# Optimization experiments

Hardware: AMD Instinct MI355X
Metric: run time of the kernel (lower is better)

The kernel has to match this reference:

```python
import jax, jax.numpy as jnp
import numpy as np

B, N, C, H = 8, 1024, 1024, 16
D = C // H
SCALE = D ** -0.5


def setup_inputs() -> dict:
    key = jax.random.key(0)
    ks = jax.random.split(key, 5)
    s = 0.02  # keep pre-softmax logits in a sane range
    return {
        "x": jax.random.normal(ks[0], (B, N, C), dtype=jnp.float32),
        "Wq": jax.random.normal(ks[1], (C, C), dtype=jnp.float32) * s,
        "bq": jax.random.normal(ks[2], (C,), dtype=jnp.float32) * s,
        "Wkv": jax.random.normal(ks[3], (C, 2 * C), dtype=jnp.float32) * s,
        "bkv": jax.random.normal(ks[4], (2 * C,), dtype=jnp.float32) * s,
    }


def reference(x, Wq, bq, Wkv, bkv):
    b, n, c = x.shape
    h, d = H, c // H
    q = (x @ Wq + bq).reshape(b, n, h, d)                 # [b,n,h,d]
    kv = x @ Wkv + bkv                                     # [b,n,2c]
    k, v = jnp.split(kv, 2, axis=-1)                       # each [b,n,c]
    k = k.reshape(b, n, h, d)
    v = v.reshape(b, n, h, d)
    att = jnp.einsum("bnhd,bmhd->bnmh", q, k) * SCALE      # [b,n,m,h]
    att = jax.nn.softmax(att, axis=2)                      # softmax over keys (m)
    out = jnp.einsum("bnmh,bmhd->bnhd", att, v).reshape(b, n, c)
    return out
```

## Files before the change

kernel.cpp:

```cpp
#include <hip/hip_runtime.h>
#include <stdint.h>

using u16 = unsigned short;
using u32 = unsigned int;
using bf16x8 = __attribute__((ext_vector_type(8))) __bf16;
using f32x4  = __attribute__((ext_vector_type(4))) float;

#define NB 8
#define NN 1024
#define NC 1024
#define NH 16
#define ND 64
#define QSCALE 0.18033688011112042f

__device__ __forceinline__ u16 f2bf(float f) {
  u32 u = __float_as_uint(f);
  return (u16)((u + 0x7fffu + ((u >> 16) & 1u)) >> 16);
}
__device__ __forceinline__ u16 bfc(float f) {
  __bf16 b = (__bf16)f;
  return __builtin_bit_cast(u16, b);
}
__device__ __forceinline__ u32 pack2(u16 a, u16 b) { return (u32)a | ((u32)b << 16); }

__device__ __forceinline__ void gload16(const void* g, void* l) {
  __builtin_amdgcn_global_load_lds((__attribute__((address_space(1))) const u32*)g,
                                   (__attribute__((address_space(3))) u32*)l, 16, 0, 0);
}

__global__ void k_prep(const float* __restrict__ x, const float* __restrict__ Wq,
                       const float* __restrict__ Wkv,
                       u16* __restrict__ xb, u16* __restrict__ Wt) {
  __shared__ u16 tile[64][72];
  int bid = blockIdx.x;
  int t = threadIdx.x;
  if (bid < 8192) {
    int i = bid * 256 + t;
    float4 v = ((const float4*)x)[i];
    ((uint2*)xb)[i] = make_uint2(pack2(f2bf(v.x), f2bf(v.y)), pack2(f2bf(v.z), f2bf(v.w)));
    return;
  }
  {
    int pb = bid - 8192;
    int k0 = (pb & 15) << 6;
    int c0 = (pb >> 4) << 6;
    bool isQ = (c0 < 1024);
    const float* src = isQ ? Wq : Wkv;
    int ldw  = isQ ? 1024 : 2048;
    int csrc = isQ ? c0 : (c0 - 1024);
    float sc = isQ ? QSCALE : 1.0f;

    int r  = t >> 2;
    int cq = (t & 3) << 4;
    const float* p = src + (size_t)(k0 + r) * ldw + csrc + cq;
#pragma unroll
    for (int j = 0; j < 16; j += 4) {
      float4 v = *(const float4*)(p + j);
      tile[r][cq + j + 0] = f2bf(v.x * sc);
      tile[r][cq + j + 1] = f2bf(v.y * sc);
      tile[r][cq + j + 2] = f2bf(v.z * sc);
      tile[r][cq + j + 3] = f2bf(v.w * sc);
    }
    __syncthreads();
    int co = t >> 2;
    int kq = (t & 3) << 4;
    u16 v0[16];
#pragma unroll
    for (int j = 0; j < 16; ++j) v0[j] = tile[kq + j][co];
    uint4 o0, o1;
    o0.x = pack2(v0[0], v0[1]);  o0.y = pack2(v0[2], v0[3]);
    o0.z = pack2(v0[4], v0[5]);  o0.w = pack2(v0[6], v0[7]);
    o1.x = pack2(v0[8], v0[9]);  o1.y = pack2(v0[10], v0[11]);
    o1.z = pack2(v0[12], v0[13]); o1.w = pack2(v0[14], v0[15]);
    u16* dst = Wt + (size_t)(c0 + co) * 1024 + k0 + kq;
    *(uint4*)dst = o0;
    *(uint4*)(dst + 8) = o1;
  }
}

__launch_bounds__(512, 2)
__global__ void k_gemm(const u16* __restrict__ A, const u16* __restrict__ Bw,
                       const float* __restrict__ bq, const float* __restrict__ bkv,
                       u16* __restrict__ qws, u16* __restrict__ kws, u16* __restrict__ vtw) {
  __shared__ __align__(16) u16 LA[2][16384];
  __shared__ __align__(16) u16 LB[2][12288];
  int flat = blockIdx.x;
  int xcd = flat & 7, idx = flat >> 3;
  int m0 = (xcd * 4 + (idx & 3)) * 256;
  int n0 = (idx >> 2) * 192;
  int tid = threadIdx.x;
  int w = tid >> 6, lane = tid & 63;
  int lo = lane & 15, hi = lane >> 4;
  int wm = w >> 2, wn = w & 3;

  f32x4 acc[8][3] = {};

  int cs = ((tid & 7) ^ ((tid >> 3) & 7)) * 8;
  const u16* Ag = A  + (size_t)(m0 + (tid >> 3)) * 1024 + cs;
  const u16* Bg = Bw + (size_t)(n0 + (tid >> 3)) * 1024 + cs;

  int ck0 = ((hi ^ (lo & 7)) << 3);
  int ck1 = (((4 + hi) ^ (lo & 7)) << 3);
  const u16* laR = &LA[0][wm * 8192 + lo * 64];
  const u16* lbR = &LB[0][(wn * 48 + lo) * 64];

#define MFMA_(a, b, c) __builtin_amdgcn_mfma_f32_16x16x32_bf16(a, b, c, 0, 0, 0)
#define SBAR() __builtin_amdgcn_sched_barrier(0); __builtin_amdgcn_s_barrier(); __builtin_amdgcn_sched_barrier(0)
#define LGKM0() asm volatile("s_waitcnt lgkmcnt(0)" ::: "memory"); __builtin_amdgcn_sched_barrier(0)

#define ST_AH(BUF, MH, KT)                                                                     \
  gload16(Ag + (size_t)((MH) * 128) * 1024 + (KT) * 64,      &LA[BUF][(MH) * 8192 + tid * 8]); \
  gload16(Ag + (size_t)((MH) * 128 + 64) * 1024 + (KT) * 64, &LA[BUF][(MH) * 8192 + 4096 + tid * 8]);
#define ST_BT(BUF, NH, KT)                                                                     \
  gload16(Bg + (size_t)((NH) * 64) * 1024 + (KT) * 64,       &LB[BUF][(NH) * 4096 + tid * 8]);

#define QUAD(Q, NI)                                                           \
  __builtin_amdgcn_s_setprio(1);                                              \
  _Pragma("unroll")                                                           \
  for (int ks = 0; ks < 2; ++ks)                                              \
    _Pragma("unroll")                                                         \
    for (int mi = 0; mi < 4; ++mi)                                            \
      acc[(Q) * 4 + mi][NI] = MFMA_(af[mi][ks], bfr[NI][ks], acc[(Q) * 4 + mi][NI]); \
  __builtin_amdgcn_s_setprio(0);

  ST_AH(0, 0, 0); ST_AH(0, 1, 0); ST_BT(0, 0, 0); ST_BT(0, 1, 0); ST_BT(0, 2, 0);
  ST_AH(1, 0, 1); ST_AH(1, 1, 1); ST_BT(1, 0, 1); ST_BT(1, 1, 1); ST_BT(1, 2, 1);
  asm volatile("s_waitcnt vmcnt(7)" ::: "memory");
  __builtin_amdgcn_s_barrier();

#pragma unroll 1
  for (int t = 0; t < 16; ++t) {
    int b = t & 1;
    const u16* la = laR + b * 16384;
    const u16* lb = lbR + b * 12288;
    bf16x8 af[4][2], bfr[3][2];
    bool st = (t < 14);

#pragma unroll
    for (int mi = 0; mi < 4; ++mi) {
      af[mi][0] = *(const bf16x8*)(la + mi * 1024 + ck0);
      af[mi][1] = *(const bf16x8*)(la + mi * 1024 + ck1);
    }
    bfr[0][0] = *(const bf16x8*)(lb + ck0);
    bfr[0][1] = *(const bf16x8*)(lb + ck1);
    SBAR();
    LGKM0();
    QUAD(0, 0);
    SBAR();

    bfr[1][0] = *(const bf16x8*)(lb + 1024 + ck0);
    bfr[1][1] = *(const bf16x8*)(lb + 1024 + ck1);
    SBAR();
    LGKM0();
    QUAD(0, 1);
    SBAR();

    bfr[2][0] = *(const bf16x8*)(lb + 2048 + ck0);
    bfr[2][1] = *(const bf16x8*)(lb + 2048 + ck1);
    SBAR();
    LGKM0();
    QUAD(0, 2);
    SBAR();

#pragma unroll
    for (int mi = 0; mi < 4; ++mi) {
      af[mi][0] = *(const bf16x8*)(la + (4 + mi) * 1024 + ck0);
      af[mi][1] = *(const bf16x8*)(la + (4 + mi) * 1024 + ck1);
    }
    if (st) { ST_BT(b, 0, t + 2); }
    SBAR();
    LGKM0();
    QUAD(1, 0);
    SBAR();

    if (st) { ST_AH(b, 0, t + 2); ST_BT(b, 1, t + 2); }
    SBAR();
    QUAD(1, 1);
    SBAR();

    if (st) { ST_AH(b, 1, t + 2); ST_BT(b, 2, t + 2); }
    SBAR();
    QUAD(1, 2);
    if (t < 14)       { asm volatile("s_waitcnt vmcnt(7)" ::: "memory"); }
    else if (t == 14) { asm volatile("s_waitcnt vmcnt(0)" ::: "memory"); }
    SBAR();
  }
#undef QUAD
#undef ST_AH
#undef ST_BT
#undef SBAR
#undef LGKM0
#undef MFMA_

#pragma unroll
  for (int ni = 0; ni < 3; ++ni) {
    int c = n0 + wn * 48 + ni * 16 + lo;
    float bvl = (c < 1024) ? bq[c] * QSCALE : bkv[c - 1024];
    if (c < 2048) {
#pragma unroll
      for (int mi = 0; mi < 8; ++mi) {
#pragma unroll
        for (int r = 0; r < 4; ++r) {
          int m = m0 + wm * 128 + mi * 16 + hi * 4 + r;
          int b = m >> 10, tok = m & 1023;
          u16 o = f2bf(acc[mi][ni][r] + bvl);
          if (c < 1024) {
            int h = c >> 6, d = c & 63;
            qws[((size_t)(b * 16 + h) * 1024 + tok) * 64 + d] = o;
          } else {
            int c2 = c - 1024; int h = c2 >> 6, d = c2 & 63;
            kws[((size_t)(b * 16 + h) * 1024 + tok) * 64 + d] = o;
          }
        }
      }
    } else {
      int c2 = c - 2048; int h = c2 >> 6, d = c2 & 63;
#pragma unroll
      for (int mi = 0; mi < 8; ++mi) {
        int m = m0 + wm * 128 + mi * 16 + hi * 4;
        int b = m >> 10, tok = m & 1023;
        ushort4 pk;
        pk.x = bfc(acc[mi][ni][0] + bvl);
        pk.y = bfc(acc[mi][ni][1] + bvl);
        pk.z = bfc(acc[mi][ni][2] + bvl);
        pk.w = bfc(acc[mi][ni][3] + bvl);
        *(ushort4*)&vtw[((size_t)(b * 16 + h) * 64 + d) * 1024 + tok] = pk;
      }
    }
  }
}

__launch_bounds__(512)
__global__ void k_attn(const u16* __restrict__ q, const u16* __restrict__ k,
                       const u16* __restrict__ vt, float* __restrict__ out) {
  __shared__ __align__(16) u16 Ks[2][4096];
  __shared__ __align__(16) u16 Vs[2][4096];
  __shared__ __align__(16) u16 P[2][8][16][72];
  int bh = blockIdx.x;
  int q0 = blockIdx.y * 256;
  int tid = threadIdx.x;
  int w = tid >> 6, lane = tid & 63;
  int lo = lane & 15, hi = lane >> 4;
  int b = bh >> 4, h = bh & 15;

  const u16* kbase = k  + (size_t)bh * 65536;
  const u16* vbase = vt + (size_t)bh * 65536;

  int srow = w * 8 + (lane >> 3);
  int cg   = (lane & 7) ^ ((lane >> 3) & 7);
  const u16* gK = kbase + (size_t)srow * 64   + cg * 8;
  const u16* gV = vbase + (size_t)srow * 1024 + cg * 8;
  u16* lK0 = &Ks[0][w * 512];
  u16* lK1 = &Ks[1][w * 512];
  u16* lV0 = &Vs[0][w * 512];
  u16* lV1 = &Vs[1][w * 512];

  const u16* qp = q + ((size_t)bh * 1024 + q0 + w * 16 + lo) * 64 + hi * 8;
  bf16x8 qfA0 = *(const bf16x8*)(qp);
  bf16x8 qfA1 = *(const bf16x8*)(qp + 32);
  bf16x8 qfB0 = *(const bf16x8*)(qp + 128 * 64);
  bf16x8 qfB1 = *(const bf16x8*)(qp + 128 * 64 + 32);

  f32x4 accA[4] = {}, accB[4] = {};
  float mA = -1e30f, lA = 0.f;
  float mB = -1e30f, lB = 0.f;

  int sw = lo & 7;

  gload16(gK, lK0);
  gload16(gV, lV0);
  __syncthreads();

  for (int t = 0; t < 16; ++t) {
    int cur = t & 1;
    if (t < 15) {
      gload16(gK + (t + 1) * 4096, cur ? lK0 : lK1);
      gload16(gV + (t + 1) * 64,   cur ? lV0 : lV1);
    }
    f32x4 sA[4] = {}, sB[4] = {};
    const u16* kb = Ks[cur];
    __builtin_amdgcn_s_setprio(1);
#pragma unroll
    for (int ni = 0; ni < 4; ++ni) {
      const u16* kp = kb + (ni * 16 + lo) * 64;
      bf16x8 kf0 = *(const bf16x8*)(kp + ((hi ^ sw) * 8));
      bf16x8 kf1 = *(const bf16x8*)(kp + (((4 + hi) ^ sw) * 8));
      sA[ni] = __builtin_amdgcn_mfma_f32_16x16x32_bf16(kf0, qfA0, sA[ni], 0, 0, 0);
      sA[ni] = __builtin_amdgcn_mfma_f32_16x16x32_bf16(kf1, qfA1, sA[ni], 0, 0, 0);
      sB[ni] = __builtin_amdgcn_mfma_f32_16x16x32_bf16(kf0, qfB0, sB[ni], 0, 0, 0);
      sB[ni] = __builtin_amdgcn_mfma_f32_16x16x32_bf16(kf1, qfB1, sB[ni], 0, 0, 0);
    }
    __builtin_amdgcn_s_setprio(0);

#define SOFTMAX(S, M, L, PI)                                                   \
    {                                                                          \
      float a0 = fmaxf(fmaxf(S[0][0], S[0][1]), fmaxf(S[0][2], S[0][3]));      \
      float a1 = fmaxf(fmaxf(S[1][0], S[1][1]), fmaxf(S[1][2], S[1][3]));      \
      float a2 = fmaxf(fmaxf(S[2][0], S[2][1]), fmaxf(S[2][2], S[2][3]));      \
      float a3 = fmaxf(fmaxf(S[3][0], S[3][1]), fmaxf(S[3][2], S[3][3]));      \
      float pm = fmaxf(fmaxf(a0, a1), fmaxf(a2, a3));                          \
      pm = fmaxf(pm, __shfl_xor(pm, 16));                                      \
      pm = fmaxf(pm, __shfl_xor(pm, 32));                                      \
      if (!__all(pm <= M + 8.0f)) {                                            \
        float mn = fmaxf(M, pm);                                               \
        float corr = __builtin_amdgcn_exp2f(M - mn);                           \
        M = mn;                                                                \
        L *= corr;                                                             \
        float cr[4];                                                           \
        _Pragma("unroll")                                                      \
        for (int r = 0; r < 4; ++r) cr[r] = __shfl(corr, hi * 4 + r);          \
        _Pragma("unroll")                                                      \
        for (int ci = 0; ci < 4; ++ci)                                         \
          _Pragma("unroll")                                                    \
          for (int r = 0; r < 4; ++r) acc##PI[ci][r] *= cr[r];                 \
      }                                                                        \
      float rs = 0.f;                                                          \
      _Pragma("unroll")                                                        \
      for (int ni = 0; ni < 4; ++ni) {                                         \
        float p0 = __builtin_amdgcn_exp2f(S[ni][0] - M);                       \
        float p1 = __builtin_amdgcn_exp2f(S[ni][1] - M);                       \
        float p2 = __builtin_amdgcn_exp2f(S[ni][2] - M);                       \
        float p3 = __builtin_amdgcn_exp2f(S[ni][3] - M);                       \
        rs += (p0 + p1) + (p2 + p3);                                           \
        ushort4 pk;                                                            \
        pk.x = bfc(p0); pk.y = bfc(p1); pk.z = bfc(p2); pk.w = bfc(p3);        \
        *(ushort4*)&P[PI##I][w][lo][ni * 16 + hi * 4] = pk;                    \
      }                                                                        \
      rs += __shfl_xor(rs, 16);                                                \
      rs += __shfl_xor(rs, 32);                                                \
      L += rs;                                                                 \
    }
#define AI 0
#define BI 1
    SOFTMAX(sA, mA, lA, A)
    SOFTMAX(sB, mB, lB, B)
#undef SOFTMAX

    bf16x8 pA0 = *(const bf16x8*)(&P[0][w][lo][hi * 8]);
    bf16x8 pA1 = *(const bf16x8*)(&P[0][w][lo][32 + hi * 8]);
    bf16x8 pB0 = *(const bf16x8*)(&P[1][w][lo][hi * 8]);
    bf16x8 pB1 = *(const bf16x8*)(&P[1][w][lo][32 + hi * 8]);
    const u16* vb = Vs[cur];
    __builtin_amdgcn_s_setprio(1);
#pragma unroll
    for (int ci = 0; ci < 4; ++ci) {
      const u16* vp = vb + (ci * 16 + lo) * 64;
      bf16x8 vf0 = *(const bf16x8*)(vp + ((hi ^ sw) * 8));
      bf16x8 vf1 = *(const bf16x8*)(vp + (((4 + hi) ^ sw) * 8));
      accA[ci] = __builtin_amdgcn_mfma_f32_16x16x32_bf16(pA0, vf0, accA[ci], 0, 0, 0);
      accA[ci] = __builtin_amdgcn_mfma_f32_16x16x32_bf16(pA1, vf1, accA[ci], 0, 0, 0);
      accB[ci] = __builtin_amdgcn_mfma_f32_16x16x32_bf16(pB0, vf0, accB[ci], 0, 0, 0);
      accB[ci] = __builtin_amdgcn_mfma_f32_16x16x32_bf16(pB1, vf1, accB[ci], 0, 0, 0);
    }
    __builtin_amdgcn_s_setprio(0);
    __syncthreads();
  }
  {
    float inv = 1.0f / lA;
    float ivr[4];
#pragma unroll
    for (int r = 0; r < 4; ++r) ivr[r] = __shfl(inv, hi * 4 + r);
#pragma unroll
    for (int r = 0; r < 4; ++r) {
      int n = q0 + w * 16 + hi * 4 + r;
      float* dst = out + ((size_t)(b * 1024 + n)) * 1024 + h * 64;
#pragma unroll
      for (int ci = 0; ci < 4; ++ci) dst[ci * 16 + lo] = accA[ci][r] * ivr[r];
    }
  }
  {
    float inv = 1.0f / lB;
    float ivr[4];
#pragma unroll
    for (int r = 0; r < 4; ++r) ivr[r] = __shfl(inv, hi * 4 + r);
#pragma unroll
    for (int r = 0; r < 4; ++r) {
      int n = q0 + 128 + w * 16 + hi * 4 + r;
      float* dst = out + ((size_t)(b * 1024 + n)) * 1024 + h * 64;
#pragma unroll
      for (int ci = 0; ci < 4; ++ci) dst[ci * 16 + lo] = accB[ci][r] * ivr[r];
    }
  }
}

extern "C" void kernel_launch(void* const* d_in, const int* in_sizes, int n_in,
                              void* d_out, int out_size, void* d_ws, size_t ws_size,
                              hipStream_t stream) {
  const float* x   = (const float*)d_in[0];
  const float* Wq  = (const float*)d_in[1];
  const float* bq  = (const float*)d_in[2];
  const float* Wkv = (const float*)d_in[3];
  const float* bkv = (const float*)d_in[4];
  float* out = (float*)d_out;

  char* ws = (char*)d_ws;
  u16*   xb   = (u16*)(ws);
  u16*   Wt   = (u16*)(ws + 16777216);
  u16*   qws  = (u16*)(ws + 23080960);
  u16*   kws  = (u16*)(ws + 39858176);
  u16*   vtw  = (u16*)(ws + 73412608);

  k_prep<<<8960, 256, 0, stream>>>(x, Wq, Wkv, xb, Wt);
  k_gemm<<<512, 512, 0, stream>>>(xb, Wt, bq, bkv, qws, kws, vtw);
  {
    dim3 g(128, 4);
    k_attn<<<g, 512, 0, stream>>>(qws, kws, vtw, out);
  }
}
```

Before: 132.5 us.

## Enlarge QKV GEMM tile to 256x384 with interleaved single-stage prefetch

Doubles the N-tile of the projection GEMM from 192 to 384 columns, so each block computes 256x384 with 48 accumulators per lane, and halves the grid to 256 blocks. The K-loop pipeline is rebuilt: the next k-tile's global-to-LDS loads are spread across the MFMA groups of the current tile, with a full vmcnt(0) wait at the end of each iteration instead of the previous two-tile-ahead staggered prefetch. The goal is higher arithmetic intensity per LDS/global byte. In exchange, LDS use grows to about 160KB and register pressure rises, which could cut occupancy. With 256 blocks on 256 CUs there is only one wave of work and no latency hiding across blocks.

```diff
diff --git a/kernel.cpp b/kernel.cpp
--- a/kernel.cpp
+++ b/kernel.cpp
@@ -83,17 +83,17 @@
                        const float* __restrict__ bq, const float* __restrict__ bkv,
                        u16* __restrict__ qws, u16* __restrict__ kws, u16* __restrict__ vtw) {
   __shared__ __align__(16) u16 LA[2][16384];
-  __shared__ __align__(16) u16 LB[2][12288];
+  __shared__ __align__(16) u16 LB[2][24576];
   int flat = blockIdx.x;
   int xcd = flat & 7, idx = flat >> 3;
   int m0 = (xcd * 4 + (idx & 3)) * 256;
-  int n0 = (idx >> 2) * 192;
+  int n0 = (idx >> 2) * 384;
   int tid = threadIdx.x;
   int w = tid >> 6, lane = tid & 63;
   int lo = lane & 15, hi = lane >> 4;
   int wm = w >> 2, wn = w & 3;
 
-  f32x4 acc[8][3] = {};
+  f32x4 acc[8][6] = {};
 
   int cs = ((tid & 7) ^ ((tid >> 3) & 7)) * 8;
   const u16* Ag = A  + (size_t)(m0 + (tid >> 3)) * 1024 + cs;
@@ -101,100 +101,71 @@
 
   int ck0 = ((hi ^ (lo & 7)) << 3);
   int ck1 = (((4 + hi) ^ (lo & 7)) << 3);
-  const u16* laR = &LA[0][wm * 8192 + lo * 64];
-  const u16* lbR = &LB[0][(wn * 48 + lo) * 64];
+  const u16* laR = &LA[0][(wm * 128 + lo) * 64];
+  const u16* lbR = &LB[0][(wn * 96 + lo) * 64];
 
 #define MFMA_(a, b, c) __builtin_amdgcn_mfma_f32_16x16x32_bf16(a, b, c, 0, 0, 0)
 #define SBAR() __builtin_amdgcn_sched_barrier(0); __builtin_amdgcn_s_barrier(); __builtin_amdgcn_sched_barrier(0)
 #define LGKM0() asm volatile("s_waitcnt lgkmcnt(0)" ::: "memory"); __builtin_amdgcn_sched_barrier(0)
 
-#define ST_AH(BUF, MH, KT)                                                                     \
-  gload16(Ag + (size_t)((MH) * 128) * 1024 + (KT) * 64,      &LA[BUF][(MH) * 8192 + tid * 8]); \
-  gload16(Ag + (size_t)((MH) * 128 + 64) * 1024 + (KT) * 64, &LA[BUF][(MH) * 8192 + 4096 + tid * 8]);
-#define ST_BT(BUF, NH, KT)                                                                     \
-  gload16(Bg + (size_t)((NH) * 64) * 1024 + (KT) * 64,       &LB[BUF][(NH) * 4096 + tid * 8]);
-
-#define QUAD(Q, NI)                                                           \
-  __builtin_amdgcn_s_setprio(1);                                              \
-  _Pragma("unroll")                                                           \
-  for (int ks = 0; ks < 2; ++ks)                                              \
-    _Pragma("unroll")                                                         \
-    for (int mi = 0; mi < 4; ++mi)                                            \
-      acc[(Q) * 4 + mi][NI] = MFMA_(af[mi][ks], bfr[NI][ks], acc[(Q) * 4 + mi][NI]); \
-  __builtin_amdgcn_s_setprio(0);
-
-  ST_AH(0, 0, 0); ST_AH(0, 1, 0); ST_BT(0, 0, 0); ST_BT(0, 1, 0); ST_BT(0, 2, 0);
-  ST_AH(1, 0, 1); ST_AH(1, 1, 1); ST_BT(1, 0, 1); ST_BT(1, 1, 1); ST_BT(1, 2, 1);
-  asm volatile("s_waitcnt vmcnt(7)" ::: "memory");
+#define ST_A(BUF, P, KT) gload16(Ag + (size_t)((P) * 64) * 1024 + (KT) * 64, &LA[BUF][(P) * 4096 + tid * 8]);
+#define ST_B(BUF, P, KT) gload16(Bg + (size_t)((P) * 64) * 1024 + (KT) * 64, &LB[BUF][(P) * 4096 + tid * 8]);
+
+  ST_A(0, 0, 0); ST_A(0, 1, 0); ST_A(0, 2, 0); ST_A(0, 3, 0);
+  ST_B(0, 0, 0); ST_B(0, 1, 0); ST_B(0, 2, 0); ST_B(0, 3, 0); ST_B(0, 4, 0); ST_B(0, 5, 0);
+  asm volatile("s_waitcnt vmcnt(0)" ::: "memory");
   __builtin_amdgcn_s_barrier();
 
 #pragma unroll 1
   for (int t = 0; t < 16; ++t) {
     int b = t & 1;
     const u16* la = laR + b * 16384;
-    const u16* lb = lbR + b * 12288;
-    bf16x8 af[4][2], bfr[3][2];
-    bool st = (t < 14);
-
-#pragma unroll
-    for (int mi = 0; mi < 4; ++mi) {
-      af[mi][0] = *(const bf16x8*)(la + mi * 1024 + ck0);
-      af[mi][1] = *(const bf16x8*)(la + mi * 1024 + ck1);
-    }
-    bfr[0][0] = *(const bf16x8*)(lb + ck0);
-    bfr[0][1] = *(const bf16x8*)(lb + ck1);
-    SBAR();
-    LGKM0();
-    QUAD(0, 0);
-    SBAR();
-
-    bfr[1][0] = *(const bf16x8*)(lb + 1024 + ck0);
-    bfr[1][1] = *(const bf16x8*)(lb + 1024 + ck1);
-    SBAR();
-    LGKM0();
-    QUAD(0, 1);
-    SBAR();
-
-    bfr[2][0] = *(const bf16x8*)(lb + 2048 + ck0);
-    bfr[2][1] = *(const bf16x8*)(lb + 2048 + ck1);
-    SBAR();
-    LGKM0();
-    QUAD(0, 2);
-    SBAR();
-
-#pragma unroll
-    for (int mi = 0; mi < 4; ++mi) {
-      af[mi][0] = *(const bf16x8*)(la + (4 + mi) * 1024 + ck0);
-      af[mi][1] = *(const bf16x8*)(la + (4 + mi) * 1024 + ck1);
-    }
-    if (st) { ST_BT(b, 0, t + 2); }
-    SBAR();
-    LGKM0();
-    QUAD(1, 0);
-    SBAR();
-
-    if (st) { ST_AH(b, 0, t + 2); ST_BT(b, 1, t + 2); }
-    SBAR();
-    QUAD(1, 1);
-    SBAR();
-
-    if (st) { ST_AH(b, 1, t + 2); ST_BT(b, 2, t + 2); }
-    SBAR();
-    QUAD(1, 2);
-    if (t < 14)       { asm volatile("s_waitcnt vmcnt(7)" ::: "memory"); }
-    else if (t == 14) { asm volatile("s_waitcnt vmcnt(0)" ::: "memory"); }
-    SBAR();
-  }
-#undef QUAD
-#undef ST_AH
-#undef ST_BT
+    const u16* lb = lbR + b * 24576;
+    bool st = (t < 15);
+    int kn = t + 1;
+
+#pragma unroll
+    for (int q = 0; q < 2; ++q) {
+      bf16x8 af[4][2];
+#pragma unroll
+      for (int mi = 0; mi < 4; ++mi) {
+        af[mi][0] = *(const bf16x8*)(la + (q * 64 + mi * 16) * 64 + ck0);
+        af[mi][1] = *(const bf16x8*)(la + (q * 64 + mi * 16) * 64 + ck1);
+      }
+#pragma unroll
+      for (int ni = 0; ni < 6; ++ni) {
+        bf16x8 bfr0 = *(const bf16x8*)(lb + ni * 1024 + ck0);
+        bf16x8 bfr1 = *(const bf16x8*)(lb + ni * 1024 + ck1);
+        if (st) {
+          if (q == 0 && ni >= 1 && ni <= 4) { ST_A(b ^ 1, ni - 1, kn); }
+          else if (q == 0 && ni == 5)       { ST_B(b ^ 1, 0, kn); }
+          else if (q == 1 && ni <= 4)       { ST_B(b ^ 1, ni + 1, kn); }
+        }
+        SBAR();
+        LGKM0();
+        __builtin_amdgcn_s_setprio(1);
+#pragma unroll
+        for (int mi = 0; mi < 4; ++mi) {
+          acc[q * 4 + mi][ni] = MFMA_(af[mi][0], bfr0, acc[q * 4 + mi][ni]);
+          acc[q * 4 + mi][ni] = MFMA_(af[mi][1], bfr1, acc[q * 4 + mi][ni]);
+        }
+        __builtin_amdgcn_s_setprio(0);
+        if (q == 1 && ni == 5) {
+          if (st) { asm volatile("s_waitcnt vmcnt(0)" ::: "memory"); }
+        }
+        SBAR();
+      }
+    }
+  }
+#undef ST_A
+#undef ST_B
 #undef SBAR
 #undef LGKM0
 #undef MFMA_
 
 #pragma unroll
-  for (int ni = 0; ni < 3; ++ni) {
-    int c = n0 + wn * 48 + ni * 16 + lo;
+  for (int ni = 0; ni < 6; ++ni) {
+    int c = n0 + wn * 96 + ni * 16 + lo;
     float bvl = (c < 1024) ? bq[c] * QSCALE : bkv[c - 1024];
     if (c < 2048) {
 #pragma unroll
@@ -401,7 +372,7 @@
   u16*   vtw  = (u16*)(ws + 73412608);
 
   k_prep<<<8960, 256, 0, stream>>>(x, Wq, Wkv, xb, Wt);
-  k_gemm<<<512, 512, 0, stream>>>(xb, Wt, bq, bkv, qws, kws, vtw);
+  k_gemm<<<256, 512, 0, stream>>>(xb, Wt, bq, bkv, qws, kws, vtw);
   {
     dim3 g(128, 4);
     k_attn<<<g, 512, 0, stream>>>(qws, kws, vtw, out);
```

New measurement: 131.3 us (median of 2 runs). No clear change (-0.9%).
